# Kernel optimization log

Measured on AMD Instinct MI355X. Metric: run time of the kernel, lower is better.

Reference implementation:

```python
import jax, jax.numpy as jnp
import numpy as np

DIM = 1024
H = 16
DH = DIM // H  # 64


def _l2norm(a):
    # matches torch F.normalize(dim=-1, eps=1e-12)
    n = jnp.linalg.norm(a, axis=-1, keepdims=True)
    return a / jnp.maximum(n, 1e-12)


def setup_inputs() -> dict:
    key = jax.random.key(0)
    ks = jax.random.split(key, 6)
    B, T = 4, 4096
    s = 0.02
    return {
        "x": jax.random.normal(ks[0], (B, T, DIM), jnp.float32),
        "Wqkv": jax.random.normal(ks[1], (3 * DIM, DIM), jnp.float32) * s,
        "Wg": jax.random.normal(ks[2], (H, DIM), jnp.float32) * s,
        "bg": jnp.zeros((H,), jnp.float32),
        "Wb": jax.random.normal(ks[3], (H, DIM), jnp.float32) * s,
        "bb": jnp.zeros((H,), jnp.float32),
        "Wout": jax.random.normal(ks[4], (DIM, DIM), jnp.float32) * s,
    }


def reference(x, Wqkv, Wg, bg, Wb, bb, Wout):
    B, T, D = x.shape
    qkv = (x @ Wqkv.T).reshape(B, T, 3, H, DH)
    q = _l2norm(qkv[:, :, 0])   # [B,T,H,Dh]
    k = _l2norm(qkv[:, :, 1])
    v = qkv[:, :, 2]
    alpha = jax.nn.sigmoid(x @ Wg.T + bg)  # [B,T,H]
    beta = jax.nn.sigmoid(x @ Wb.T + bb)   # [B,T,H]

    # time-major for scan
    qT = jnp.moveaxis(q, 1, 0)  # [T,B,H,Dh]
    kT = jnp.moveaxis(k, 1, 0)
    vT = jnp.moveaxis(v, 1, 0)
    aT = jnp.moveaxis(alpha, 1, 0)  # [T,B,H]
    bT = jnp.moveaxis(beta, 1, 0)

    S0 = jnp.zeros((B, H, DH, DH), jnp.float32)

    def step(S, inp):
        q_t, k_t, v_t, a_t, b_t = inp
        Sk = jnp.einsum('bhij,bhj->bhi', S, k_t)          # S @ k_t
        a = a_t[..., None, None]
        b = b_t[..., None, None]
        # S = a * (S - b * (S k) k^T) + b * v k^T
        S = a * (S - b * Sk[..., :, None] * k_t[..., None, :]) \
            + b * v_t[..., :, None] * k_t[..., None, :]
        o = jnp.einsum('bhij,bhj->bhi', S, q_t)
        return S, o

    _, outs = jax.lax.scan(step, S0, (qT, kT, vT, aT, bT))  # [T,B,H,Dh]
    out = jnp.moveaxis(outs, 0, 1).reshape(B, T, D)
    return out @ Wout.T
```

## Files before the change

### kernel.cpp

```cpp
#include <hip/hip_runtime.h>
#include <hip/hip_bf16.h>

#define NB   4
#define NT   4096
#define BT   16384
#define NDIM 1024
#define NH   16
#define NDH  64
#define CC   64
#define NCH  (NT / CC)
#define NPAIR 64
#define NU   (NPAIR * NCH)
#define DBS  24

using u16 = unsigned short;
typedef __bf16 bf16x8 __attribute__((ext_vector_type(8)));
typedef float f32x4 __attribute__((ext_vector_type(4)));
typedef unsigned short u16x8 __attribute__((ext_vector_type(8)));
typedef unsigned short u16x4 __attribute__((ext_vector_type(4)));

__device__ __forceinline__ float bf2f(u16 b) { return __uint_as_float(((unsigned)b) << 16); }
__device__ __forceinline__ u16 f2bf(float f) {
  return __builtin_bit_cast(u16, __float2bfloat16(f));
}
__device__ __forceinline__ int swz(int row, int e) { return e ^ ((row & 7) << 3); }
__device__ __forceinline__ bf16x8 zfrag() {
  u16x8 z = {0, 0, 0, 0, 0, 0, 0, 0};
  return __builtin_bit_cast(bf16x8, z);
}
__device__ __forceinline__ long qkvT_idx(int s, int h, long bt, int d) {
  return ((long)(s * 16 + h) * BT + bt) * 64 + d;
}

__global__ __launch_bounds__(256) void k_f32_to_bf16(const float* __restrict__ in,
                                                     u16* __restrict__ out, long n4) {
  long i = (long)blockIdx.x * blockDim.x + threadIdx.x;
  if (i >= n4) return;
  float4 f = reinterpret_cast<const float4*>(in)[i];
  u16x4 o;
  o.x = f2bf(f.x); o.y = f2bf(f.y); o.z = f2bf(f.z); o.w = f2bf(f.w);
  reinterpret_cast<u16x4*>(out)[i] = o;
}

__global__ __launch_bounds__(256) void k_build_wgb(const float* __restrict__ Wg,
                                                   const float* __restrict__ Wb,
                                                   u16* __restrict__ out) {
  int i = blockIdx.x * 256 + threadIdx.x;
  int row = i >> 10, col = i & 1023;
  float f = 0.f;
  if (row < 16)       f = Wg[row * 1024 + col];
  else if (row < 32)  f = Wb[(row - 16) * 1024 + col];
  out[i] = f2bf(f);
}

typedef unsigned int u32_as1 __attribute__((address_space(1)));
typedef unsigned int u32_as3 __attribute__((address_space(3)));
__device__ __forceinline__ void gload_lds16(const void* g, void* l) {
  __builtin_amdgcn_global_load_lds((const u32_as1*)g, (u32_as3*)l, 16, 0, 0);
}

template <typename OutT>
__global__ __launch_bounds__(256) void k_gemm_bt(const u16* __restrict__ A,
                                                 const u16* __restrict__ B,
                                                 OutT* __restrict__ C,
                                                 int M, int N, int K) {
  constexpr int BM = 128, BN = 128, BK = 32;
  __shared__ __align__(16) u16 As[BM * BK];
  __shared__ __align__(16) u16 Bs[BN * BK];
  const int tid = threadIdx.x;
  const int l = tid & 63, w = tid >> 6;
  const int tn = blockIdx.x, tm = blockIdx.y;
  const long a0 = (long)tm * BM * K;
  const long b0 = (long)tn * BN * K;
  const int srow = tid >> 2;
  const int scol = (tid & 3) << 3;
  const int wrow = (w >> 1) << 6;
  const int wcol = (w & 1) << 6;
  const int fr = l & 15, fq = l >> 4;

  f32x4 acc[4][4];
#pragma unroll
  for (int m = 0; m < 4; ++m)
#pragma unroll
    for (int n = 0; n < 4; ++n) acc[m][n] = f32x4{0.f, 0.f, 0.f, 0.f};

  for (int kk = 0; kk < K; kk += BK) {
    __syncthreads();
    const u16* gA = A + a0 + (long)srow * K + kk + scol;
    const u16* gB = B + b0 + (long)srow * K + kk + scol;
    gload_lds16(gA,                &As[(w * 16) * BK]);
    gload_lds16(gA + 64 * (long)K, &As[(64 + w * 16) * BK]);
    gload_lds16(gB,                &Bs[(w * 16) * BK]);
    gload_lds16(gB + 64 * (long)K, &Bs[(64 + w * 16) * BK]);
    __syncthreads();

    bf16x8 af[4], bfv[4];
#pragma unroll
    for (int m = 0; m < 4; ++m)
      af[m] = *(const bf16x8*)&As[(wrow + m * 16 + fr) * BK + (fq << 3)];
#pragma unroll
    for (int n = 0; n < 4; ++n)
      bfv[n] = *(const bf16x8*)&Bs[(wcol + n * 16 + fr) * BK + (fq << 3)];
#pragma unroll
    for (int m = 0; m < 4; ++m)
#pragma unroll
      for (int n = 0; n < 4; ++n)
        acc[m][n] = __builtin_amdgcn_mfma_f32_16x16x32_bf16(af[m], bfv[n], acc[m][n], 0, 0, 0);
  }

#pragma unroll
  for (int m = 0; m < 4; ++m) {
#pragma unroll
    for (int n = 0; n < 4; ++n) {
      const int r0 = tm * BM + wrow + m * 16 + fq * 4;
      const int c  = tn * BN + wcol + n * 16 + fr;
#pragma unroll
      for (int r = 0; r < 4; ++r) {
        float v = acc[m][n][r];
        long idx = (long)(r0 + r) * N + c;
        if constexpr (sizeof(OutT) == 2) C[idx] = f2bf(v);
        else                             C[idx] = v;
      }
    }
  }
}

template <typename OutT, bool QKVT>
__global__ __launch_bounds__(512, 2) void k_gemm256(const u16* __restrict__ A,
                                                    const u16* __restrict__ B,
                                                    OutT* __restrict__ C,
                                                    int M, int N, int K) {
  __shared__ __align__(16) u16 As[2][2][256 * 32];
  __shared__ __align__(16) u16 Bs[2][2][256 * 32];
  const int tid = threadIdx.x;
  const int l = tid & 63, w = tid >> 6;
  const int wm = w >> 2, wn = w & 3;
  const int fr = l & 15, fq = l >> 4;
  const int nwg = gridDim.x;
  const int cpx = nwg >> 3;
  const int bid = blockIdx.x;
  const int sbid = (bid & 7) * cpx + (bid >> 3);
  const int ntn = N >> 8;
  const int tm = sbid / ntn, tn = sbid - tm * ntn;
  const long a0 = (long)tm * 256 * K;
  const long b0 = (long)tn * 256 * K;
  const int srow0 = tid >> 2;
  const int scol8 = (((tid & 3) ^ ((tid >> 4) & 3)) << 3);
  const int cswz = ((fq ^ ((fr >> 2) & 3)) << 3);
  const int NKT = K >> 6;

  auto stage_half = [&](int kt, int buf, int hf) {
    const int ks = hf >> 1;
    const u16* Gp = (hf & 1) ? B : A;
    const long g0 = ((hf & 1) ? b0 : a0) + (long)kt * 64 + ks * 32 + scol8;
    u16* lb = (hf & 1) ? &Bs[buf][ks][w * 512] : &As[buf][ks][w * 512];
#pragma unroll
    for (int r = 0; r < 2; ++r)
      gload_lds16(Gp + g0 + (long)(r * 128 + srow0) * K, lb + r * 4096);
  };

  f32x4 acc[8][4];
#pragma unroll
  for (int m = 0; m < 8; ++m)
#pragma unroll
    for (int n = 0; n < 4; ++n) acc[m][n] = f32x4{0.f, 0.f, 0.f, 0.f};

  stage_half(0, 0, 0); stage_half(0, 0, 1); stage_half(0, 0, 2); stage_half(0, 0, 3);

  for (int kt = 0; kt < NKT; ++kt) {
    const int bi = kt & 1;
    const bool pf = (kt + 1 < NKT);
    asm volatile("s_waitcnt vmcnt(4)" ::: "memory");
    __builtin_amdgcn_sched_barrier(0);
    __builtin_amdgcn_s_barrier();
    __builtin_amdgcn_sched_barrier(0);
    {
      const u16* ap = &As[bi][0][(wm * 128 + fr) * 32 + cswz];
      const u16* bp = &Bs[bi][0][(wn * 64 + fr) * 32 + cswz];
      bf16x8 bfr[4], afr[4];
#pragma unroll
      for (int n = 0; n < 4; ++n) bfr[n] = *(const bf16x8*)(bp + n * 512);
#pragma unroll
      for (int m = 0; m < 4; ++m) afr[m] = *(const bf16x8*)(ap + m * 512);
      if (pf) stage_half(kt + 1, bi ^ 1, 0);
      __builtin_amdgcn_s_setprio(1);
#pragma unroll
      for (int m = 0; m < 4; ++m)
#pragma unroll
        for (int n = 0; n < 4; ++n)
          acc[m][n] = __builtin_amdgcn_mfma_f32_16x16x32_bf16(afr[m], bfr[n], acc[m][n], 0, 0, 0);
      __builtin_amdgcn_s_setprio(0);
#pragma unroll
      for (int m = 0; m < 4; ++m) afr[m] = *(const bf16x8*)(ap + (4 + m) * 512);
      if (pf) stage_half(kt + 1, bi ^ 1, 1);
      __builtin_amdgcn_s_setprio(1);
#pragma unroll
      for (int m = 0; m < 4; ++m)
#pragma unroll
        for (int n = 0; n < 4; ++n)
          acc[4 + m][n] = __builtin_amdgcn_mfma_f32_16x16x32_bf16(afr[m], bfr[n], acc[4 + m][n], 0, 0, 0);
      __builtin_amdgcn_s_setprio(0);
    }
    if (pf) { asm volatile("s_waitcnt vmcnt(4)" ::: "memory"); }
    else    { asm volatile("s_waitcnt vmcnt(0)" ::: "memory"); }
    __builtin_amdgcn_sched_barrier(0);
    __builtin_amdgcn_s_barrier();
    __builtin_amdgcn_sched_barrier(0);
    {
      const u16* ap = &As[bi][1][(wm * 128 + fr) * 32 + cswz];
      const u16* bp = &Bs[bi][1][(wn * 64 + fr) * 32 + cswz];
      bf16x8 bfr[4], afr[4];
#pragma unroll
      for (int n = 0; n < 4; ++n) bfr[n] = *(const bf16x8*)(bp + n * 512);
#pragma unroll
      for (int m = 0; m < 4; ++m) afr[m] = *(const bf16x8*)(ap + m * 512);
      if (pf) stage_half(kt + 1, bi ^ 1, 2);
      __builtin_amdgcn_s_setprio(1);
#pragma unroll
      for (int m = 0; m < 4; ++m)
#pragma unroll
        for (int n = 0; n < 4; ++n)
          acc[m][n] = __builtin_amdgcn_mfma_f32_16x16x32_bf16(afr[m], bfr[n], acc[m][n], 0, 0, 0);
      __builtin_amdgcn_s_setprio(0);
#pragma unroll
      for (int m = 0; m < 4; ++m) afr[m] = *(const bf16x8*)(ap + (4 + m) * 512);
      if (pf) stage_half(kt + 1, bi ^ 1, 3);
      __builtin_amdgcn_s_setprio(1);
#pragma unroll
      for (int m = 0; m < 4; ++m)
#pragma unroll
        for (int n = 0; n < 4; ++n)
          acc[4 + m][n] = __builtin_amdgcn_mfma_f32_16x16x32_bf16(afr[m], bfr[n], acc[4 + m][n], 0, 0, 0);
      __builtin_amdgcn_s_setprio(0);
    }
  }

#pragma unroll
  for (int m = 0; m < 8; ++m)
#pragma unroll
    for (int n = 0; n < 4; ++n) {
      const int row0 = tm * 256 + wm * 128 + m * 16 + fq * 4;
      const int col  = tn * 256 + wn * 64 + n * 16 + fr;
#pragma unroll
      for (int r = 0; r < 4; ++r) {
        if constexpr (QKVT) {
          const int hb = (tn * 256 + wn * 64) >> 6;
          long idx = ((long)hb * BT + (row0 + r)) * 64 + (n * 16 + fr);
          C[idx] = (OutT)f2bf(acc[m][n][r]);
        } else {
          long idx = (long)(row0 + r) * N + col;
          if constexpr (sizeof(OutT) == 2) C[idx] = f2bf(acc[m][n][r]);
          else                             C[idx] = acc[m][n][r];
        }
      }
    }
}

__global__ __launch_bounds__(256) void k_gates_fin(const float* __restrict__ raw,
                                                   const float* __restrict__ bg,
                                                   const float* __restrict__ bb,
                                                   float* __restrict__ alpha,
                                                   float* __restrict__ beta) {
  int i = blockIdx.x * 256 + threadIdx.x;
  if (i >= BT * NH) return;
  int bt = i >> 4, h = i & 15;
  float ga = raw[(long)bt * 128 + h] + bg[h];
  float gb = raw[(long)bt * 128 + 16 + h] + bb[h];
  alpha[i] = 1.f / (1.f + __expf(-ga));
  beta[i]  = 1.f / (1.f + __expf(-gb));
}

__global__ __launch_bounds__(256, 3) void k_prep(u16* __restrict__ qkv,
                                                 const float* __restrict__ alpha,
                                                 const float* __restrict__ beta,
                                                 float* __restrict__ A63G,
                                                 u16* __restrict__ oi) {
  __shared__ __align__(16) u16 Ks[64 * 64];
  __shared__ __align__(16) u16 WTs[128 * 64];
  __shared__ __align__(16) u16 Lb[64 * 64];
  __shared__ __align__(16) u16 MqS[64 * 64];
  __shared__ __align__(16) u16 KdT[64 * 64];
  __shared__ __align__(16) u16 Db[4 * 16 * DBS];
  __shared__ float cvec[64], Avec[64], bvec[64], nkinv[64], nqinv[64];

  const int unit = blockIdx.x;
  const int pair = unit >> 6, ch = unit & 63;
  const int b = pair >> 4, h = pair & 15;
  const int tid = threadIdx.x, l = tid & 63, w = tid >> 6;
  const int fr = l & 15, fq = l >> 4;
  const long t0 = (long)b * NT + (long)ch * CC;

  u16x8 kreg[2], vreg[2], qreg[2];
  int srow_[2], sseg_[2];
#pragma unroll
  for (int p = 0; p < 2; ++p) {
    int idx = p * 256 + tid;
    srow_[p] = idx >> 3; sseg_[p] = (idx & 7) * 8;
    qreg[p] = *(const u16x8*)&qkv[qkvT_idx(0, h, t0 + srow_[p], sseg_[p])];
    kreg[p] = *(const u16x8*)&qkv[qkvT_idx(1, h, t0 + srow_[p], sseg_[p])];
    vreg[p] = *(const u16x8*)&qkv[qkvT_idx(2, h, t0 + srow_[p], sseg_[p])];
  }
  const int ar = w * 16 + fr;
  u16x8 qa[2];
#pragma unroll
  for (int kk = 0; kk < 2; ++kk)
    qa[kk] = *(const u16x8*)&qkv[qkvT_idx(0, h, t0 + ar, kk * 32 + fq * 8)];

  if (w == 0) {
    float av = alpha[(t0 + l) * 16 + h];
    float bv = beta[(t0 + l) * 16 + h];
    float cl = __log2f(av);
#pragma unroll
    for (int d = 1; d < 64; d <<= 1) {
      float up = __shfl_up(cl, d);
      if (l >= d) cl += up;
    }
    float A = exp2f(cl);
    cvec[l] = cl; Avec[l] = A; bvec[l] = bv;
    if (l == 63) A63G[unit] = A;
  }
  __syncthreads();

#pragma unroll
  for (int p = 0; p < 2; ++p) {
    int row = srow_[p], seg = sseg_[p];
    *(u16x8*)&Ks[row * 64 + swz(row, seg)] = kreg[p];
    float kss = 0.f, qss = 0.f;
    const float bs = bvec[row];
#pragma unroll
    for (int e = 0; e < 8; ++e) {
      float kf = bf2f(kreg[p][e]), qf = bf2f(qreg[p][e]);
      kss += kf * kf; qss += qf * qf;
      int c = seg + e;
      WTs[c * 64 + swz(c, row)] = f2bf(bs * bf2f(vreg[p][e]));
    }
    kss += __shfl_xor(kss, 1); kss += __shfl_xor(kss, 2); kss += __shfl_xor(kss, 4);
    qss += __shfl_xor(qss, 1); qss += __shfl_xor(qss, 2); qss += __shfl_xor(qss, 4);
    if ((tid & 7) == 0) { nkinv[row] = kss; nqinv[row] = qss; }
  }
  __syncthreads();

  if (tid < 64)       nkinv[tid] = rsqrtf(fmaxf(nkinv[tid], 1e-24f));
  else if (tid < 128) nqinv[tid - 64] = rsqrtf(fmaxf(nqinv[tid - 64], 1e-24f));
  __syncthreads();

  f32x4 akk[4], aqk[4];
#pragma unroll
  for (int n = 0; n < 4; ++n) { akk[n] = f32x4{0, 0, 0, 0}; aqk[n] = f32x4{0, 0, 0, 0}; }
  {
    bf16x8 afK[2], afQ[2];
#pragma unroll
    for (int kk = 0; kk < 2; ++kk) {
      afK[kk] = __builtin_bit_cast(bf16x8, *(const u16x8*)&Ks[ar * 64 + swz(ar, kk * 32 + fq * 8)]);
      afQ[kk] = __builtin_bit_cast(bf16x8, qa[kk]);
    }
#pragma unroll
    for (int n = 0; n < 4; ++n) {
      const int br = n * 16 + fr;
#pragma unroll
      for (int kk = 0; kk < 2; ++kk) {
        bf16x8 bk = __builtin_bit_cast(bf16x8, *(const u16x8*)&Ks[br * 64 + swz(br, kk * 32 + fq * 8)]);
        akk[n] = __builtin_amdgcn_mfma_f32_16x16x32_bf16(afK[kk], bk, akk[n], 0, 0, 0);
        aqk[n] = __builtin_amdgcn_mfma_f32_16x16x32_bf16(afQ[kk], bk, aqk[n], 0, 0, 0);
      }
    }
  }
  {
    const int j = tid & 63, tg4 = tid >> 6;
    const float c63 = cvec[63];
    u16 kb[16], kd[16];
#pragma unroll
    for (int tt = 0; tt < 16; ++tt) {
      int t = tg4 * 16 + tt;
      float kv = bf2f(Ks[t * 64 + swz(t, j)]) * nkinv[t];
      kb[tt] = f2bf(bvec[t] * Avec[t] * kv);
      kd[tt] = f2bf(exp2f(c63 - cvec[t]) * kv);
    }
#pragma unroll
    for (int g8 = 0; g8 < 2; ++g8) {
      u16x8 o1, o2;
#pragma unroll
      for (int e = 0; e < 8; ++e) { o1[e] = kb[g8 * 8 + e]; o2[e] = kd[g8 * 8 + e]; }
      int colg = tg4 * 16 + g8 * 8;
      *(u16x8*)&WTs[(64 + j) * 64 + swz(64 + j, colg)] = o1;
      *(u16x8*)&KdT[j * 64 + swz(j, colg)] = o2;
    }
  }
#pragma unroll
  for (int n = 0; n < 4; ++n)
#pragma unroll
    for (int r = 0; r < 4; ++r) {
      const int t = w * 16 + fq * 4 + r;
      const int s = n * 16 + fr;
      const float e = exp2f(cvec[t] - cvec[s]);
      Lb[t * 64 + swz(t, s)] = (s < t) ? f2bf(bvec[t] * e * nkinv[t] * nkinv[s] * akk[n][r]) : (u16)0;
      MqS[t * 64 + swz(t, s)] = (s <= t) ? f2bf(e * nqinv[t] * nkinv[s] * aqk[n][r]) : (u16)0;
    }
  __syncthreads();

  if (l < 16) {
    const int c = l;
    const int rb = w * 16;
    float x[16];
#pragma unroll
    for (int u = 0; u < 16; ++u) {
      float a2 = (u == c) ? 1.f : 0.f;
#pragma unroll
      for (int s = 0; s < u; ++s)
        a2 -= bf2f(Lb[(rb + u) * 64 + swz(rb + u, rb + s)]) * x[s];
      x[u] = a2;
    }
#pragma unroll
    for (int u = 0; u < 16; ++u)
      Db[w * 16 * DBS + u * DBS + c] = f2bf(x[u]);
  }
  __syncthreads();

  float ltil[6];
  {
    const int pbi[6] = {1, 2, 2, 3, 3, 3}, pbj[6] = {0, 0, 1, 0, 1, 2};
    const int tt = tid >> 4, s = tid & 15;
#pragma unroll
    for (int e = 0; e < 6; ++e) {
      int bi = pbi[e], bj = pbj[e];
      float a2 = 0.f;
#pragma unroll
      for (int u = 0; u < 16; ++u)
        a2 += bf2f(Db[bi * 16 * DBS + tt * DBS + u]) *
              bf2f(Lb[(bi * 16 + u) * 64 + swz(bi * 16 + u, bj * 16 + s)]);
      ltil[e] = a2;
    }
  }
  f32x4 rtacc[2][4];
#pragma unroll
  for (int rt2 = 0; rt2 < 2; ++rt2) {
    const int rrow = (w * 2 + rt2) * 16 + fr;
#pragma unroll
    for (int bi = 0; bi < 4; ++bi) {
      bf16x8 a2 = (fq < 2)
        ? __builtin_bit_cast(bf16x8, *(const u16x8*)&WTs[rrow * 64 + swz(rrow, bi * 16 + fq * 8)])
        : zfrag();
      bf16x8 b2 = (fq < 2)
        ? __builtin_bit_cast(bf16x8, *(const u16x8*)&Db[bi * 16 * DBS + fr * DBS + fq * 8])
        : zfrag();
      rtacc[rt2][bi] = __builtin_amdgcn_mfma_f32_16x16x32_bf16(a2, b2, f32x4{0, 0, 0, 0}, 0, 0, 0);
    }
  }
  __syncthreads();
  {
    const int pbi[6] = {1, 2, 2, 3, 3, 3}, pbj[6] = {0, 0, 1, 0, 1, 2};
    const int tt = tid >> 4, s = tid & 15;
#pragma unroll
    for (int e = 0; e < 6; ++e)
      Lb[(pbi[e] * 16 + tt) * 64 + swz(pbi[e] * 16 + tt, pbj[e] * 16 + s)] = f2bf(-ltil[e]);
  }
#pragma unroll
  for (int rt2 = 0; rt2 < 2; ++rt2)
#pragma unroll
    for (int bi = 0; bi < 4; ++bi)
#pragma unroll
      for (int r = 0; r < 4; ++r) {
        int rr = (w * 2 + rt2) * 16 + fq * 4 + r;
        WTs[rr * 64 + swz(rr, bi * 16 + fr)] = f2bf(rtacc[rt2][bi][r]);
      }
  __syncthreads();

#pragma unroll
  for (int rt2 = 0; rt2 < 2; ++rt2) {
    const int rrow = (w * 2 + rt2) * 16 + fr;
    const int wr0 = (w * 2 + rt2) * 16 + fq * 4;
#pragma unroll
    for (int i = 1; i < 4; ++i) {
      f32x4 a2;
#pragma unroll
      for (int r = 0; r < 4; ++r)
        a2[r] = bf2f(WTs[(wr0 + r) * 64 + swz(wr0 + r, i * 16 + fr)]);
      {
        bf16x8 af = __builtin_bit_cast(bf16x8, *(const u16x8*)&WTs[rrow * 64 + swz(rrow, fq * 8)]);
        bf16x8 bf_;
        if (i == 1) bf_ = (fq < 2)
          ? __builtin_bit_cast(bf16x8, *(const u16x8*)&Lb[(16 + fr) * 64 + swz(16 + fr, fq * 8)])
          : zfrag();
        else bf_ = __builtin_bit_cast(bf16x8, *(const u16x8*)&Lb[(i * 16 + fr) * 64 + swz(i * 16 + fr, fq * 8)]);
        a2 = __builtin_amdgcn_mfma_f32_16x16x32_bf16(af, bf_, a2, 0, 0, 0);
      }
      if (i == 3) {
        bf16x8 af = __builtin_bit_cast(bf16x8, *(const u16x8*)&WTs[rrow * 64 + swz(rrow, 32 + fq * 8)]);
        bf16x8 bf_ = (fq < 2)
          ? __builtin_bit_cast(bf16x8, *(const u16x8*)&Lb[(48 + fr) * 64 + swz(48 + fr, 32 + fq * 8)])
          : zfrag();
        a2 = __builtin_amdgcn_mfma_f32_16x16x32_bf16(af, bf_, a2, 0, 0, 0);
      }
#pragma unroll
      for (int r = 0; r < 4; ++r)
        WTs[(wr0 + r) * 64 + swz(wr0 + r, i * 16 + fr)] = f2bf(a2[r]);
    }
  }
  __syncthreads();

  u16 qpre[4][4];
#pragma unroll
  for (int n = 0; n < 4; ++n)
#pragma unroll
    for (int r = 0; r < 4; ++r)
      qpre[n][r] = qkv[qkvT_idx(0, h, t0 + w * 16 + fq * 4 + r, n * 16 + fr)];

  f32x4 aG[4], aU[4], aQe[4], aOi[4];
#pragma unroll
  for (int n = 0; n < 4; ++n) {
    aG[n] = f32x4{0, 0, 0, 0}; aU[n] = f32x4{0, 0, 0, 0};
    aQe[n] = f32x4{0, 0, 0, 0}; aOi[n] = f32x4{0, 0, 0, 0};
  }
  {
    bf16x8 aKd[2], aWv[2], aMq[2];
#pragma unroll
    for (int kk = 0; kk < 2; ++kk) {
      aKd[kk] = __builtin_bit_cast(bf16x8, *(const u16x8*)&KdT[ar * 64 + swz(ar, kk * 32 + fq * 8)]);
      aWv[kk] = __builtin_bit_cast(bf16x8, *(const u16x8*)&WTs[ar * 64 + swz(ar, kk * 32 + fq * 8)]);
      aMq[kk] = __builtin_bit_cast(bf16x8, *(const u16x8*)&MqS[ar * 64 + swz(ar, kk * 32 + fq * 8)]);
    }
#pragma unroll
    for (int n = 0; n < 4; ++n) {
      const int br = n * 16 + fr;
#pragma unroll
      for (int kk = 0; kk < 2; ++kk) {
        bf16x8 bTw = __builtin_bit_cast(bf16x8, *(const u16x8*)&WTs[(64 + br) * 64 + swz(64 + br, kk * 32 + fq * 8)]);
        bf16x8 bKd = __builtin_bit_cast(bf16x8, *(const u16x8*)&KdT[br * 64 + swz(br, kk * 32 + fq * 8)]);
        bf16x8 bWv = __builtin_bit_cast(bf16x8, *(const u16x8*)&WTs[br * 64 + swz(br, kk * 32 + fq * 8)]);
        aG[n]  = __builtin_amdgcn_mfma_f32_16x16x32_bf16(aKd[kk], bTw, aG[n], 0, 0, 0);
        aU[n]  = __builtin_amdgcn_mfma_f32_16x16x32_bf16(aWv[kk], bKd, aU[n], 0, 0, 0);
        aQe[n] = __builtin_amdgcn_mfma_f32_16x16x32_bf16(aMq[kk], bTw, aQe[n], 0, 0, 0);
        aOi[n] = __builtin_amdgcn_mfma_f32_16x16x32_bf16(aMq[kk], bWv, aOi[n], 0, 0, 0);
      }
    }
  }
  asm volatile("s_waitcnt vmcnt(0)" ::: "memory");
  __builtin_amdgcn_sched_barrier(0);
#pragma unroll
  for (int n = 0; n < 4; ++n)
#pragma unroll
    for (int r = 0; r < 4; ++r) {
      const int i = w * 16 + fq * 4 + r;
      const int cn = n * 16 + fr;
      const int sw = swz(i, cn);
      qkv[qkvT_idx(0, h, t0 + i, sw)] = f2bf(Avec[i] * nqinv[i] * bf2f(qpre[n][r]) - aQe[n][r]);
      qkv[qkvT_idx(1, h, t0 + i, sw)] = f2bf(-aG[n][r]);
      qkv[qkvT_idx(2, h, t0 + i, sw)] = f2bf(aU[n][r]);
      Ks[i * 64 + cn] = f2bf(aOi[n][r]);
    }
  __syncthreads();
#pragma unroll
  for (int p = 0; p < 2; ++p) {
    const int idx = p * 256 + tid;
    const int row = idx >> 3, seg = (idx & 7) * 8;
    *(u16x8*)&oi[(long)unit * 4096 + row * 64 + seg] = *(const u16x8*)&Ks[row * 64 + seg];
  }
}

__global__ __launch_bounds__(1024) void k_seq(const u16* __restrict__ qkv,
                                              const u16* __restrict__ oi,
                                              const float* __restrict__ A63G,
                                              u16* __restrict__ ob) {
  __shared__ __align__(16) u16 Sb[64 * 64];
  __shared__ __align__(16) u16 Obs[64 * 64];
  __shared__ __align__(16) u16 stg[2][4][64 * 64];
  __shared__ float a63s[64];
  const int pair = blockIdx.x;
  const int b = pair >> 4, h = pair & 15;
  const int tid = threadIdx.x, l = tid & 63, w = tid >> 6;
  const int fr = l & 15, fq = l >> 4;
  const int tw = w >> 2, td = w & 3;

  auto stage = [&](int c, int bi) {
    const long tg = (long)b * NT + (long)c * CC;
    if (tid < 512) {
      const int row = tid >> 3, seg = (tid & 7) * 8;
#pragma unroll
      for (int m = 0; m < 4; ++m) {
        const u16* src = (m < 3)
          ? &qkv[qkvT_idx(m, h, tg + row, seg)]
          : &oi[(long)(pair * 64 + c) * 4096 + row * 64 + seg];
        gload_lds16(src, &stg[bi][m][row * 64 + seg]);
      }
    }
  };

  if (tid < 64) a63s[tid] = A63G[pair * 64 + tid];
  for (int i = tid; i < 4096; i += 1024) Sb[i] = 0;
  stage(0, 0);
  f32x4 sacc = f32x4{0, 0, 0, 0};
  asm volatile("s_waitcnt lgkmcnt(0)" ::: "memory");
  __builtin_amdgcn_sched_barrier(0);

  for (int c = 0; c < NCH; ++c) {
    const int bi = c & 1;
    const long tg = (long)b * NT + (long)c * CC;
    if (c + 1 < NCH) {
      stage(c + 1, bi ^ 1);
      asm volatile("s_waitcnt vmcnt(4)" ::: "memory");
    } else {
      asm volatile("s_waitcnt vmcnt(0)" ::: "memory");
    }
    __builtin_amdgcn_sched_barrier(0);
    __builtin_amdgcn_s_barrier();
    __builtin_amdgcn_sched_barrier(0);

    const u16* Qe = stg[bi][0];
    const u16* Gm = stg[bi][1];
    const u16* Um = stg[bi][2];
    const u16* Obl = stg[bi][3];

    const int at = tw * 16 + fr;
    const int bd = td * 16 + fr;
    f32x4 ao = f32x4{0, 0, 0, 0};
    const float A63 = a63s[c];
#pragma unroll
    for (int r = 0; r < 4; ++r) sacc[r] *= A63;
#pragma unroll
    for (int kk = 0; kk < 2; ++kk) {
      bf16x8 aq = __builtin_bit_cast(bf16x8, *(const u16x8*)&Qe[at * 64 + swz(at, kk * 32 + fq * 8)]);
      bf16x8 sb = __builtin_bit_cast(bf16x8, *(const u16x8*)&Sb[bd * 64 + swz(bd, kk * 32 + fq * 8)]);
      ao = __builtin_amdgcn_mfma_f32_16x16x32_bf16(aq, sb, ao, 0, 0, 0);
      bf16x8 as_ = __builtin_bit_cast(bf16x8, *(const u16x8*)&Sb[at * 64 + swz(at, kk * 32 + fq * 8)]);
      bf16x8 g  = __builtin_bit_cast(bf16x8, *(const u16x8*)&Gm[bd * 64 + swz(bd, kk * 32 + fq * 8)]);
      sacc = __builtin_amdgcn_mfma_f32_16x16x32_bf16(as_, g, sacc, 0, 0, 0);
    }
#pragma unroll
    for (int r = 0; r < 4; ++r) {
      const int ri = tw * 16 + fq * 4 + r;
      const int cj = td * 16 + fr;
      sacc[r] += bf2f(Um[ri * 64 + swz(ri, cj)]);
      Obs[ri * 64 + cj] = f2bf(bf2f(Obl[ri * 64 + cj]) + ao[r]);
    }
    asm volatile("s_waitcnt lgkmcnt(0)" ::: "memory");
    __builtin_amdgcn_s_barrier();
#pragma unroll
    for (int r = 0; r < 4; ++r) {
      const int d = tw * 16 + fq * 4 + r, j = td * 16 + fr;
      Sb[d * 64 + swz(d, j)] = f2bf(sacc[r]);
    }
    if (tid < 512) {
      const int row = tid >> 3, seg = (tid & 7) * 8;
      *(u16x8*)&ob[(tg + row) * 1024 + h * 64 + seg] = *(const u16x8*)&Obs[row * 64 + seg];
    }
    asm volatile("s_waitcnt lgkmcnt(0)" ::: "memory");
    __builtin_amdgcn_sched_barrier(0);
  }
}

extern "C" void kernel_launch(void* const* d_in, const int* in_sizes, int n_in,
                              void* d_out, int out_size, void* d_ws, size_t ws_size,
                              hipStream_t stream) {
  const float* x    = (const float*)d_in[0];
  const float* Wqkv = (const float*)d_in[1];
  const float* Wg   = (const float*)d_in[2];
  const float* bg   = (const float*)d_in[3];
  const float* Wb   = (const float*)d_in[4];
  const float* bb   = (const float*)d_in[5];
  const float* Wout = (const float*)d_in[6];
  float* out = (float*)d_out;

  char* ws = (char*)d_ws;
  u16* xb    = (u16*)ws;
  u16* wqkvb = xb    + (long)BT * NDIM;
  u16* woutb = wqkvb + (long)3072 * 1024;
  u16* wgbb  = woutb + (long)1024 * 1024;
  u16* qkvb  = wgbb  + (long)128 * 1024;
  u16* ob    = qkvb  + (long)BT * 3072;
  float* graw  = (float*)(ob + (long)BT * NDIM);
  float* alpha = graw + (long)BT * 128;
  float* beta  = alpha + (long)BT * NH;
  float* A63G  = graw;
  u16*   oi    = xb;

  k_f32_to_bf16<<<(BT * (long)NDIM / 4 + 255) / 256, 256, 0, stream>>>(x, xb, BT * (long)NDIM / 4);
  k_f32_to_bf16<<<(3072L * 1024 / 4 + 255) / 256, 256, 0, stream>>>(Wqkv, wqkvb, 3072L * 1024 / 4);
  k_f32_to_bf16<<<(1024L * 1024 / 4 + 255) / 256, 256, 0, stream>>>(Wout, woutb, 1024L * 1024 / 4);
  k_build_wgb<<<(128 * 1024) / 256, 256, 0, stream>>>(Wg, Wb, wgbb);

  k_gemm256<u16, true><<<64 * 12, 512, 0, stream>>>(xb, wqkvb, qkvb, BT, 3072, NDIM);

  k_gemm_bt<float><<<dim3(1, BT / 128), 256, 0, stream>>>(xb, wgbb, graw, BT, 128, NDIM);
  k_gates_fin<<<(BT * NH + 255) / 256, 256, 0, stream>>>(graw, bg, bb, alpha, beta);

  k_prep<<<NU, 256, 0, stream>>>(qkvb, alpha, beta, A63G, oi);
  k_seq<<<NPAIR, 1024, 0, stream>>>(qkvb, oi, A63G, ob);

  k_gemm256<float, false><<<64 * 4, 512, 0, stream>>>(ob, woutb, out, BT, NDIM, NDIM);
}
```

Before: 388.4 us.

## Fuse gate GEMM with sigmoid, triple-buffer sequential scan, cut exp2 calls in prep

Replaces the 128-wide gate GEMM and its separate sigmoid kernel with one fused kernel that computes only the 32 needed gate columns and writes alpha and beta directly. The sequential per-head scan kernel now uses triple-buffered staging with a prefetch distance of two chunks, and double-buffers the state and output tiles. This removes one barrier per chunk and defers each output-tile store to the next iteration. The prep kernel precomputes exp2(-c) so pairwise decay factors become multiplies instead of exp2 calls, and its global stores are regrouped. The risks are the extra LDS use in the scan kernel and the hand-tuned vmcnt counts, which must match the new load schedule exactly.

Result: faster. 362.9 us (-6.6%).

```diff
diff --git a/kernel.cpp b/kernel.cpp
--- a/kernel.cpp
+++ b/kernel.cpp
@@ -57,72 +57,6 @@
 typedef unsigned int u32_as3 __attribute__((address_space(3)));
 __device__ __forceinline__ void gload_lds16(const void* g, void* l) {
   __builtin_amdgcn_global_load_lds((const u32_as1*)g, (u32_as3*)l, 16, 0, 0);
-}
-
-template <typename OutT>
-__global__ __launch_bounds__(256) void k_gemm_bt(const u16* __restrict__ A,
-                                                 const u16* __restrict__ B,
-                                                 OutT* __restrict__ C,
-                                                 int M, int N, int K) {
-  constexpr int BM = 128, BN = 128, BK = 32;
-  __shared__ __align__(16) u16 As[BM * BK];
-  __shared__ __align__(16) u16 Bs[BN * BK];
-  const int tid = threadIdx.x;
-  const int l = tid & 63, w = tid >> 6;
-  const int tn = blockIdx.x, tm = blockIdx.y;
-  const long a0 = (long)tm * BM * K;
-  const long b0 = (long)tn * BN * K;
-  const int srow = tid >> 2;
-  const int scol = (tid & 3) << 3;
-  const int wrow = (w >> 1) << 6;
-  const int wcol = (w & 1) << 6;
-  const int fr = l & 15, fq = l >> 4;
-
-  f32x4 acc[4][4];
-#pragma unroll
-  for (int m = 0; m < 4; ++m)
-#pragma unroll
-    for (int n = 0; n < 4; ++n) acc[m][n] = f32x4{0.f, 0.f, 0.f, 0.f};
-
-  for (int kk = 0; kk < K; kk += BK) {
-    __syncthreads();
-    const u16* gA = A + a0 + (long)srow * K + kk + scol;
-    const u16* gB = B + b0 + (long)srow * K + kk + scol;
-    gload_lds16(gA,                &As[(w * 16) * BK]);
-    gload_lds16(gA + 64 * (long)K, &As[(64 + w * 16) * BK]);
-    gload_lds16(gB,                &Bs[(w * 16) * BK]);
-    gload_lds16(gB + 64 * (long)K, &Bs[(64 + w * 16) * BK]);
-    __syncthreads();
-
-    bf16x8 af[4], bfv[4];
-#pragma unroll
-    for (int m = 0; m < 4; ++m)
-      af[m] = *(const bf16x8*)&As[(wrow + m * 16 + fr) * BK + (fq << 3)];
-#pragma unroll
-    for (int n = 0; n < 4; ++n)
-      bfv[n] = *(const bf16x8*)&Bs[(wcol + n * 16 + fr) * BK + (fq << 3)];
-#pragma unroll
-    for (int m = 0; m < 4; ++m)
-#pragma unroll
-      for (int n = 0; n < 4; ++n)
-        acc[m][n] = __builtin_amdgcn_mfma_f32_16x16x32_bf16(af[m], bfv[n], acc[m][n], 0, 0, 0);
-  }
-
-#pragma unroll
-  for (int m = 0; m < 4; ++m) {
-#pragma unroll
-    for (int n = 0; n < 4; ++n) {
-      const int r0 = tm * BM + wrow + m * 16 + fq * 4;
-      const int c  = tn * BN + wcol + n * 16 + fr;
-#pragma unroll
-      for (int r = 0; r < 4; ++r) {
-        float v = acc[m][n][r];
-        long idx = (long)(r0 + r) * N + c;
-        if constexpr (sizeof(OutT) == 2) C[idx] = f2bf(v);
-        else                             C[idx] = v;
-      }
-    }
-  }
 }
 
 template <typename OutT, bool QKVT>
@@ -256,18 +190,70 @@
     }
 }
 
-__global__ __launch_bounds__(256) void k_gates_fin(const float* __restrict__ raw,
-                                                   const float* __restrict__ bg,
-                                                   const float* __restrict__ bb,
-                                                   float* __restrict__ alpha,
-                                                   float* __restrict__ beta) {
-  int i = blockIdx.x * 256 + threadIdx.x;
-  if (i >= BT * NH) return;
-  int bt = i >> 4, h = i & 15;
-  float ga = raw[(long)bt * 128 + h] + bg[h];
-  float gb = raw[(long)bt * 128 + 16 + h] + bb[h];
-  alpha[i] = 1.f / (1.f + __expf(-ga));
-  beta[i]  = 1.f / (1.f + __expf(-gb));
+__global__ __launch_bounds__(256) void k_gates(const u16* __restrict__ xb,
+                                               const u16* __restrict__ wgb,
+                                               const float* __restrict__ bg,
+                                               const float* __restrict__ bb,
+                                               float* __restrict__ alpha,
+                                               float* __restrict__ beta) {
+  __shared__ __align__(16) u16 As[128 * 64];
+  __shared__ __align__(16) u16 Bs[32 * 64];
+  const int tid = threadIdx.x, l = tid & 63, w = tid >> 6;
+  const int fr = l & 15, fq = l >> 4;
+  const int tm = blockIdx.x;
+  const long a0 = (long)tm * 128 * 1024;
+
+  f32x4 acc[2][2];
+#pragma unroll
+  for (int m = 0; m < 2; ++m)
+#pragma unroll
+    for (int n = 0; n < 2; ++n) acc[m][n] = f32x4{0.f, 0.f, 0.f, 0.f};
+
+  for (int kk = 0; kk < 1024; kk += 64) {
+    __syncthreads();
+#pragma unroll
+    for (int p = 0; p < 4; ++p) {
+      const int idx = p * 256 + tid;
+      const int row = idx >> 3;
+      const int c8 = ((idx & 7) ^ (row & 7)) << 3;
+      gload_lds16(&xb[a0 + (long)row * 1024 + kk + c8], &As[p * 2048 + w * 512]);
+    }
+    {
+      const int row = tid >> 3;
+      const int c8 = ((tid & 7) ^ (row & 7)) << 3;
+      gload_lds16(&wgb[(long)row * 1024 + kk + c8], &Bs[w * 512]);
+    }
+    asm volatile("s_waitcnt vmcnt(0)" ::: "memory");
+    __syncthreads();
+#pragma unroll
+    for (int ks = 0; ks < 2; ++ks) {
+      bf16x8 af[2], bfv[2];
+#pragma unroll
+      for (int m = 0; m < 2; ++m) {
+        const int row = w * 32 + m * 16 + fr;
+        af[m] = __builtin_bit_cast(bf16x8, *(const u16x8*)&As[row * 64 + swz(row, ks * 32 + fq * 8)]);
+      }
+#pragma unroll
+      for (int n = 0; n < 2; ++n) {
+        const int row = n * 16 + fr;
+        bfv[n] = __builtin_bit_cast(bf16x8, *(const u16x8*)&Bs[row * 64 + swz(row, ks * 32 + fq * 8)]);
+      }
+#pragma unroll
+      for (int m = 0; m < 2; ++m)
+#pragma unroll
+        for (int n = 0; n < 2; ++n)
+          acc[m][n] = __builtin_amdgcn_mfma_f32_16x16x32_bf16(af[m], bfv[n], acc[m][n], 0, 0, 0);
+    }
+  }
+  const float bgv = bg[fr], bbv = bb[fr];
+#pragma unroll
+  for (int m = 0; m < 2; ++m)
+#pragma unroll
+    for (int r = 0; r < 4; ++r) {
+      const long row = (long)tm * 128 + w * 32 + m * 16 + fq * 4 + r;
+      alpha[row * 16 + fr] = 1.f / (1.f + __expf(-(acc[m][0][r] + bgv)));
+      beta[row * 16 + fr]  = 1.f / (1.f + __expf(-(acc[m][1][r] + bbv)));
+    }
 }
 
 __global__ __launch_bounds__(256, 3) void k_prep(u16* __restrict__ qkv,
@@ -281,7 +267,7 @@
   __shared__ __align__(16) u16 MqS[64 * 64];
   __shared__ __align__(16) u16 KdT[64 * 64];
   __shared__ __align__(16) u16 Db[4 * 16 * DBS];
-  __shared__ float cvec[64], Avec[64], bvec[64], nkinv[64], nqinv[64];
+  __shared__ float cvec[64], Avec[64], Ainvv[64], bvec[64], nkinv[64], nqinv[64];
 
   const int unit = blockIdx.x;
   const int pair = unit >> 6, ch = unit & 63;
@@ -316,7 +302,7 @@
       if (l >= d) cl += up;
     }
     float A = exp2f(cl);
-    cvec[l] = cl; Avec[l] = A; bvec[l] = bv;
+    cvec[l] = cl; Avec[l] = A; Ainvv[l] = exp2f(-cl); bvec[l] = bv;
     if (l == 63) A63G[unit] = A;
   }
   __syncthreads();
@@ -367,14 +353,14 @@
   }
   {
     const int j = tid & 63, tg4 = tid >> 6;
-    const float c63 = cvec[63];
+    const float A63v = Avec[63];
     u16 kb[16], kd[16];
 #pragma unroll
     for (int tt = 0; tt < 16; ++tt) {
       int t = tg4 * 16 + tt;
       float kv = bf2f(Ks[t * 64 + swz(t, j)]) * nkinv[t];
       kb[tt] = f2bf(bvec[t] * Avec[t] * kv);
-      kd[tt] = f2bf(exp2f(c63 - cvec[t]) * kv);
+      kd[tt] = f2bf(A63v * Ainvv[t] * kv);
     }
 #pragma unroll
     for (int g8 = 0; g8 < 2; ++g8) {
@@ -392,7 +378,7 @@
     for (int r = 0; r < 4; ++r) {
       const int t = w * 16 + fq * 4 + r;
       const int s = n * 16 + fr;
-      const float e = exp2f(cvec[t] - cvec[s]);
+      const float e = Avec[t] * Ainvv[s];
       Lb[t * 64 + swz(t, s)] = (s < t) ? f2bf(bvec[t] * e * nkinv[t] * nkinv[s] * akk[n][r]) : (u16)0;
       MqS[t * 64 + swz(t, s)] = (s <= t) ? f2bf(e * nqinv[t] * nkinv[s] * aqk[n][r]) : (u16)0;
     }
@@ -537,17 +523,25 @@
   asm volatile("s_waitcnt vmcnt(0)" ::: "memory");
   __builtin_amdgcn_sched_barrier(0);
 #pragma unroll
-  for (int n = 0; n < 4; ++n)
-#pragma unroll
-    for (int r = 0; r < 4; ++r) {
-      const int i = w * 16 + fq * 4 + r;
-      const int cn = n * 16 + fr;
-      const int sw = swz(i, cn);
-      qkv[qkvT_idx(0, h, t0 + i, sw)] = f2bf(Avec[i] * nqinv[i] * bf2f(qpre[n][r]) - aQe[n][r]);
-      qkv[qkvT_idx(1, h, t0 + i, sw)] = f2bf(-aG[n][r]);
-      qkv[qkvT_idx(2, h, t0 + i, sw)] = f2bf(aU[n][r]);
-      Ks[i * 64 + cn] = f2bf(aOi[n][r]);
-    }
+  for (int r = 0; r < 4; ++r) {
+    const int i = w * 16 + fq * 4 + r;
+#pragma unroll
+    for (int n = 0; n < 4; ++n)
+      qkv[qkvT_idx(0, h, t0 + i, swz(i, n * 16 + fr))] =
+        f2bf(Avec[i] * nqinv[i] * bf2f(qpre[n][r]) - aQe[n][r]);
+    __builtin_amdgcn_sched_barrier(0);
+#pragma unroll
+    for (int n = 0; n < 4; ++n)
+      qkv[qkvT_idx(1, h, t0 + i, swz(i, n * 16 + fr))] = f2bf(-aG[n][r]);
+    __builtin_amdgcn_sched_barrier(0);
+#pragma unroll
+    for (int n = 0; n < 4; ++n)
+      qkv[qkvT_idx(2, h, t0 + i, swz(i, n * 16 + fr))] = f2bf(aU[n][r]);
+    __builtin_amdgcn_sched_barrier(0);
+#pragma unroll
+    for (int n = 0; n < 4; ++n)
+      Ks[i * 64 + n * 16 + fr] = f2bf(aOi[n][r]);
+  }
   __syncthreads();
 #pragma unroll
   for (int p = 0; p < 2; ++p) {
@@ -561,9 +555,9 @@
                                               const u16* __restrict__ oi,
                                               const float* __restrict__ A63G,
                                               u16* __restrict__ ob) {
-  __shared__ __align__(16) u16 Sb[64 * 64];
-  __shared__ __align__(16) u16 Obs[64 * 64];
-  __shared__ __align__(16) u16 stg[2][4][64 * 64];
+  __shared__ __align__(16) u16 Sb[2][64 * 64];
+  __shared__ __align__(16) u16 Obs[2][64 * 64];
+  __shared__ __align__(16) u16 stg[3][4][64 * 64];
   __shared__ float a63s[64];
   const int pair = blockIdx.x;
   const int b = pair >> 4, h = pair & 15;
@@ -571,7 +565,8 @@
   const int fr = l & 15, fq = l >> 4;
   const int tw = w >> 2, td = w & 3;
 
-  auto stage = [&](int c, int bi) {
+  auto stage = [&](int c) {
+    const int s = c % 3;
     const long tg = (long)b * NT + (long)c * CC;
     if (tid < 512) {
       const int row = tid >> 3, seg = (tid & 7) * 8;
@@ -580,35 +575,38 @@
         const u16* src = (m < 3)
           ? &qkv[qkvT_idx(m, h, tg + row, seg)]
           : &oi[(long)(pair * 64 + c) * 4096 + row * 64 + seg];
-        gload_lds16(src, &stg[bi][m][row * 64 + seg]);
+        gload_lds16(src, &stg[s][m][row * 64 + seg]);
       }
     }
   };
 
   if (tid < 64) a63s[tid] = A63G[pair * 64 + tid];
-  for (int i = tid; i < 4096; i += 1024) Sb[i] = 0;
-  stage(0, 0);
+  for (int i = tid; i < 4096; i += 1024) Sb[0][i] = 0;
+  stage(0); stage(1);
   f32x4 sacc = f32x4{0, 0, 0, 0};
   asm volatile("s_waitcnt lgkmcnt(0)" ::: "memory");
   __builtin_amdgcn_sched_barrier(0);
 
   for (int c = 0; c < NCH; ++c) {
-    const int bi = c & 1;
+    const int sb = c & 1, st = c % 3;
     const long tg = (long)b * NT + (long)c * CC;
-    if (c + 1 < NCH) {
-      stage(c + 1, bi ^ 1);
-      asm volatile("s_waitcnt vmcnt(4)" ::: "memory");
-    } else {
-      asm volatile("s_waitcnt vmcnt(0)" ::: "memory");
-    }
+    if (c <= 1)             { asm volatile("s_waitcnt vmcnt(4)" ::: "memory"); }
+    else if (c < NCH - 1)   { asm volatile("s_waitcnt vmcnt(5)" ::: "memory"); }
+    else                    { asm volatile("s_waitcnt vmcnt(1)" ::: "memory"); }
     __builtin_amdgcn_sched_barrier(0);
     __builtin_amdgcn_s_barrier();
     __builtin_amdgcn_sched_barrier(0);
 
-    const u16* Qe = stg[bi][0];
-    const u16* Gm = stg[bi][1];
-    const u16* Um = stg[bi][2];
-    const u16* Obl = stg[bi][3];
+    if (c > 0 && tid < 512) {
+      const int row = tid >> 3, seg = (tid & 7) * 8;
+      *(u16x8*)&ob[(tg - CC + row) * 1024 + h * 64 + seg] = *(const u16x8*)&Obs[sb ^ 1][row * 64 + seg];
+    }
+    if (c + 2 < NCH) stage(c + 2);
+
+    const u16* Qe = stg[st][0];
+    const u16* Gm = stg[st][1];
+    const u16* Um = stg[st][2];
+    const u16* Obl = stg[st][3];
 
     const int at = tw * 16 + fr;
     const int bd = td * 16 + fr;
@@ -619,9 +617,9 @@
 #pragma unroll
     for (int kk = 0; kk < 2; ++kk) {
       bf16x8 aq = __builtin_bit_cast(bf16x8, *(const u16x8*)&Qe[at * 64 + swz(at, kk * 32 + fq * 8)]);
-      bf16x8 sb = __builtin_bit_cast(bf16x8, *(const u16x8*)&Sb[bd * 64 + swz(bd, kk * 32 + fq * 8)]);
-      ao = __builtin_amdgcn_mfma_f32_16x16x32_bf16(aq, sb, ao, 0, 0, 0);
-      bf16x8 as_ = __builtin_bit_cast(bf16x8, *(const u16x8*)&Sb[at * 64 + swz(at, kk * 32 + fq * 8)]);
+      bf16x8 sbf = __builtin_bit_cast(bf16x8, *(const u16x8*)&Sb[sb][bd * 64 + swz(bd, kk * 32 + fq * 8)]);
+      ao = __builtin_amdgcn_mfma_f32_16x16x32_bf16(aq, sbf, ao, 0, 0, 0);
+      bf16x8 as_ = __builtin_bit_cast(bf16x8, *(const u16x8*)&Sb[sb][at * 64 + swz(at, kk * 32 + fq * 8)]);
       bf16x8 g  = __builtin_bit_cast(bf16x8, *(const u16x8*)&Gm[bd * 64 + swz(bd, kk * 32 + fq * 8)]);
       sacc = __builtin_amdgcn_mfma_f32_16x16x32_bf16(as_, g, sacc, 0, 0, 0);
     }
@@ -630,21 +628,17 @@
       const int ri = tw * 16 + fq * 4 + r;
       const int cj = td * 16 + fr;
       sacc[r] += bf2f(Um[ri * 64 + swz(ri, cj)]);
-      Obs[ri * 64 + cj] = f2bf(bf2f(Obl[ri * 64 + cj]) + ao[r]);
+      Obs[sb][ri * 64 + cj] = f2bf(bf2f(Obl[ri * 64 + cj]) + ao[r]);
+      Sb[sb ^ 1][ri * 64 + swz(ri, cj)] = f2bf(sacc[r]);
     }
     asm volatile("s_waitcnt lgkmcnt(0)" ::: "memory");
-    __builtin_amdgcn_s_barrier();
-#pragma unroll
-    for (int r = 0; r < 4; ++r) {
-      const int d = tw * 16 + fq * 4 + r, j = td * 16 + fr;
-      Sb[d * 64 + swz(d, j)] = f2bf(sacc[r]);
-    }
-    if (tid < 512) {
-      const int row = tid >> 3, seg = (tid & 7) * 8;
-      *(u16x8*)&ob[(tg + row) * 1024 + h * 64 + seg] = *(const u16x8*)&Obs[row * 64 + seg];
-    }
-    asm volatile("s_waitcnt lgkmcnt(0)" ::: "memory");
-    __builtin_amdgcn_sched_barrier(0);
+    __builtin_amdgcn_sched_barrier(0);
+  }
+  __builtin_amdgcn_s_barrier();
+  if (tid < 512) {
+    const int row = tid >> 3, seg = (tid & 7) * 8;
+    const long tg = (long)b * NT + (long)(NCH - 1) * CC;
+    *(u16x8*)&ob[(tg + row) * 1024 + h * 64 + seg] = *(const u16x8*)&Obs[(NCH - 1) & 1][row * 64 + seg];
   }
 }
 
@@ -680,8 +674,7 @@
 
   k_gemm256<u16, true><<<64 * 12, 512, 0, stream>>>(xb, wqkvb, qkvb, BT, 3072, NDIM);
 
-  k_gemm_bt<float><<<dim3(1, BT / 128), 256, 0, stream>>>(xb, wgbb, graw, BT, 128, NDIM);
-  k_gates_fin<<<(BT * NH + 255) / 256, 256, 0, stream>>>(graw, bg, bb, alpha, beta);
+  k_gates<<<BT / 128, 256, 0, stream>>>(xb, wgbb, bg, bb, alpha, beta);
 
   k_prep<<<NU, 256, 0, stream>>>(qkvb, alpha, beta, A63G, oi);
   k_seq<<<NPAIR, 1024, 0, stream>>>(qkvb, oi, A63G, ob);
```
